# Optimization experiments

Measured on AMD Instinct MI355X. Metric: run time of the kernel, lower is better.

Reference implementation:

```python
import jax, jax.numpy as jnp
import numpy as np

# Dimensions (see shape_source): batched instruction states.
B, P, D, H, NOPS = 16384, 8, 64, 128, 37
OP_START = 16            # opcode one-hot lives in channels [16, 16+37)
DIV, MOD = 3, 4          # opcode ids for the iterative div/mod paths
CARRY_OPS = (0, 1, 2, 10, 11, 12, 13)  # ADD,SUB,MUL,LT,GT,LE,GE
NITER = 16               # div/mod iteration FFN count (source: ModuleList of 16)
NCASCADE = 7             # carry cascade iterations (source: for _ in range(7))


def setup_inputs() -> dict:
    key = jax.random.key(0)
    ks = jax.random.split(key, 20)
    s = 0.05
    n = lambda k, shape: jax.random.normal(k, shape, dtype=jnp.float32) * s
    return {
        "x": jax.random.normal(ks[0], (B, P, D), dtype=jnp.float32),
        # initial_experts (per-opcode FFN bank)
        "Wi1": n(ks[1], (NOPS, D, H)), "bi1": jnp.zeros((NOPS, H), jnp.float32),
        "Wi2": n(ks[2], (NOPS, H, D)), "bi2": jnp.zeros((NOPS, D), jnp.float32),
        # carry_attn QKV projections
        "Wq": n(ks[3], (D, D)), "Wk": n(ks[4], (D, D)), "Wv": n(ks[5], (D, D)),
        # carry_experts (per-opcode FFN bank used in the 7-iter cascade)
        "Wc1": n(ks[6], (NOPS, D, H)), "bc1": jnp.zeros((NOPS, H), jnp.float32),
        "Wc2": n(ks[7], (NOPS, H, D)), "bc2": jnp.zeros((NOPS, D), jnp.float32),
        # 16 distinct DivIterFFN layers
        "Wd1": n(ks[8], (NITER, D, H)), "bd1": jnp.zeros((NITER, H), jnp.float32),
        "Wd2": n(ks[9], (NITER, H, D)), "bd2": jnp.zeros((NITER, D), jnp.float32),
        # 16 distinct ModIterFFN layers
        "Wm1": n(ks[10], (NITER, D, H)), "bm1": jnp.zeros((NITER, H), jnp.float32),
        "Wm2": n(ks[11], (NITER, H, D)), "bm2": jnp.zeros((NITER, D), jnp.float32),
        # final_experts (per-opcode FFN bank)
        "Wf1": n(ks[12], (NOPS, D, H)), "bf1": jnp.zeros((NOPS, H), jnp.float32),
        "Wf2": n(ks[13], (NOPS, H, D)), "bf2": jnp.zeros((NOPS, D), jnp.float32),
    }


def _moe(x, op, W1, b1, W2, b2):
    """Opcode-routed expert FFN with residual: each batch element uses its opcode's weights."""
    h = jax.nn.relu(jnp.einsum('bpd,bdh->bph', x, W1[op]) + b1[op][:, None, :])
    return x + jnp.einsum('bph,bhd->bpd', h, W2[op]) + b2[op][:, None, :]


def _attn(x, Wq, Wk, Wv):
    """Carry-propagation attention across the 8 nibble positions, residual."""
    q, k, v = x @ Wq, x @ Wk, x @ Wv
    s = jax.nn.softmax(jnp.einsum('bpd,bqd->bpq', q, k) * (1.0 / np.sqrt(D)), axis=-1)
    return x + jnp.einsum('bpq,bqd->bpd', s, v)


def reference(x, Wi1, bi1, Wi2, bi2, Wq, Wk, Wv, Wc1, bc1, Wc2, bc2,
              Wd1, bd1, Wd2, bd2, Wm1, bm1, Wm2, bm2, Wf1, bf1, Wf2, bf2):
    # opcode routing: argmax over the one-hot opcode slice at position 0
    op = jnp.argmax(x[:, 0, OP_START:OP_START + NOPS], axis=-1)  # [B] int
    # Stage 1: initial opcode-routed experts
    x = _moe(x, op, Wi1, bi1, Wi2, bi2)
    carry_mask = jnp.any(op[:, None] == jnp.asarray(CARRY_OPS)[None, :], axis=1)[:, None, None]
    for _ in range(NCASCADE):
        y = _moe(_attn(x, Wq, Wk, Wv), op, Wc1, bc1, Wc2, bc2)
        x = jnp.where(carry_mask, y, x)
    # 16 iterative DIV FFNs (distinct weights per iteration), masked to DIV rows
    div_mask = (op == DIV)[:, None, None]
    for i in range(NITER):
        h = jax.nn.relu(jnp.einsum('bpd,dh->bph', x, Wd1[i]) + bd1[i])
        x = jnp.where(div_mask, x + jnp.einsum('bph,hd->bpd', h, Wd2[i]) + bd2[i], x)
    # 16 iterative MOD FFNs, masked to MOD rows
    mod_mask = (op == MOD)[:, None, None]
    for i in range(NITER):
        h = jax.nn.relu(jnp.einsum('bpd,dh->bph', x, Wm1[i]) + bm1[i])
        x = jnp.where(mod_mask, x + jnp.einsum('bph,hd->bpd', h, Wm2[i]) + bm2[i], x)
    # Stage 4: finalization experts (opcode-routed)
    x = _moe(x, op, Wf1, bf1, Wf2, bf2)
    return x
```

## Files before the change

### kernel.cpp

```cpp
#include <hip/hip_runtime.h>
#include <math.h>


typedef __bf16 bfrag __attribute__((ext_vector_type(8)));
typedef float f32x4 __attribute__((ext_vector_type(4)));

#define MFMA16(a,b,c) __builtin_amdgcn_mfma_f32_16x16x32_bf16((a),(b),(c),0,0,0)

constexpr int NB = 16384, NOPS = 37, OP_START = 16;

constexpr int WS_OPARR  = 0;
constexpr int WS_CNT    = 16384;
constexpr int WS_OFF    = 16448;
constexpr int WS_CUR    = 16512;
constexpr int WS_TB     = 16560;
constexpr int WS_ROWIDX = 16640;
constexpr int WS_INTS   = 33024;

constexpr int OFF_QKVT = 0;
constexpr int OFF_WI1T = 12288;
constexpr int OFF_WI2T = 315392;
constexpr int OFF_WC1T = 618496;
constexpr int OFF_WC2T = 921600;
constexpr int OFF_WF1T = 1224704;
constexpr int OFF_WF2T = 1527808;
constexpr int OFF_WD1T = 1830912;
constexpr int OFF_WD2T = 1961984;
constexpr int OFF_WM1T = 2093056;
constexpr int OFF_WM2T = 2224128;


__global__ void k_zero(int* cnt, int* cur) {
    int t = threadIdx.x;
    if (t < NOPS) { cnt[t] = 0; cur[t] = 0; }
}

__global__ void k_op(const float* __restrict__ x, int* __restrict__ opArr, int* __restrict__ cnt) {
    int b = blockIdx.x * 64 + threadIdx.x;
    const float4* p = (const float4*)(x + (size_t)b * 512 + OP_START);
    float best = -1e30f; int op = 0;
    #pragma unroll
    for (int j = 0; j < 9; ++j) {
        float4 v = p[j];
        int k = j * 4;
        if (v.x > best) { best = v.x; op = k; }
        if (v.y > best) { best = v.y; op = k + 1; }
        if (v.z > best) { best = v.z; op = k + 2; }
        if (v.w > best) { best = v.w; op = k + 3; }
    }
    float last = x[(size_t)b * 512 + OP_START + 36];
    if (last > best) op = 36;
    opArr[b] = op;
    atomicAdd(&cnt[op], 1);
}

__global__ void k_scan(const int* __restrict__ cnt, int* __restrict__ off, int* __restrict__ tb) {
    if (threadIdx.x == 0) {
        int a = 0, t = 0;
        for (int o = 0; o < NOPS; ++o) {
            off[o] = a; a += cnt[o];
            tb[o] = t;  t += (cnt[o] + 3) >> 2;
        }
        off[NOPS] = a; tb[NOPS] = t;
    }
}

__global__ void k_scatter(const int* __restrict__ opArr, const int* __restrict__ off,
                          int* __restrict__ cur, int* __restrict__ rowIdx) {
    __shared__ int h[NOPS], bb[NOPS];
    int tid = threadIdx.x;
    if (tid < NOPS) h[tid] = 0;
    __syncthreads();
    int b = blockIdx.x * 256 + tid;
    int op = opArr[b];
    int my = atomicAdd(&h[op], 1);
    __syncthreads();
    if (tid < NOPS && h[tid] > 0) bb[tid] = atomicAdd(&cur[tid], h[tid]);
    __syncthreads();
    rowIdx[off[op] + bb[op] + my] = b;
}

__global__ void k_tilemap(const int* __restrict__ cnt, const int* __restrict__ tb,
                          int* __restrict__ tileArr) {
    int o = blockIdx.x;
    int n = (cnt[o] + 3) >> 2, base = tb[o];
    for (int t = threadIdx.x; t < n; t += 64)
        tileArr[base + t] = (o << 12) | t;
}

__global__ void k_wt(const float* __restrict__ Wi1, const float* __restrict__ Wi2,
                     const float* __restrict__ Wq,  const float* __restrict__ Wk,
                     const float* __restrict__ Wv,
                     const float* __restrict__ Wc1, const float* __restrict__ Wc2,
                     const float* __restrict__ Wd1, const float* __restrict__ Wd2,
                     const float* __restrict__ Wm1, const float* __restrict__ Wm2,
                     const float* __restrict__ Wf1, const float* __restrict__ Wf2,
                     __bf16* __restrict__ wb) {
    __shared__ float t[8320];
    int m = blockIdx.x;
    const float* src; __bf16* dst; int R, C;
    if      (m < 37)  { src = Wi1 + m * 8192;        dst = wb + OFF_WI1T + m * 8192;        R = 64;  C = 128; }
    else if (m < 74)  { src = Wi2 + (m-37) * 8192;   dst = wb + OFF_WI2T + (m-37) * 8192;   R = 128; C = 64;  }
    else if (m < 111) { src = Wc1 + (m-74) * 8192;   dst = wb + OFF_WC1T + (m-74) * 8192;   R = 64;  C = 128; }
    else if (m < 148) { src = Wc2 + (m-111) * 8192;  dst = wb + OFF_WC2T + (m-111) * 8192;  R = 128; C = 64;  }
    else if (m < 185) { src = Wf1 + (m-148) * 8192;  dst = wb + OFF_WF1T + (m-148) * 8192;  R = 64;  C = 128; }
    else if (m < 222) { src = Wf2 + (m-185) * 8192;  dst = wb + OFF_WF2T + (m-185) * 8192;  R = 128; C = 64;  }
    else if (m < 238) { src = Wd1 + (m-222) * 8192;  dst = wb + OFF_WD1T + (m-222) * 8192;  R = 64;  C = 128; }
    else if (m < 254) { src = Wd2 + (m-238) * 8192;  dst = wb + OFF_WD2T + (m-238) * 8192;  R = 128; C = 64;  }
    else if (m < 270) { src = Wm1 + (m-254) * 8192;  dst = wb + OFF_WM1T + (m-254) * 8192;  R = 64;  C = 128; }
    else if (m < 286) { src = Wm2 + (m-270) * 8192;  dst = wb + OFF_WM2T + (m-270) * 8192;  R = 128; C = 64;  }
    else { const float* q3[3] = {Wq, Wk, Wv}; src = q3[m-286]; dst = wb + OFF_QKVT + (m-286) * 4096; R = 64; C = 64; }
    int n = R * C, Cp = C + 1;
    int logC = (C == 128) ? 7 : 6, logR = (R == 128) ? 7 : 6;
    for (int i = threadIdx.x; i < n; i += 256)
        t[(i >> logC) * Cp + (i & (C - 1))] = src[i];
    __syncthreads();
    for (int o = threadIdx.x; o < n; o += 256) {
        int c = o >> logR, r = o & (R - 1);
        dst[o] = (__bf16)t[r * Cp + c];
    }
}


__device__ __forceinline__ bfrag cvt8(const float* p) {
    float4 a = *(const float4*)p;
    float4 b = *(const float4*)(p + 4);
    bfrag r;
    r[0] = (__bf16)a.x; r[1] = (__bf16)a.y; r[2] = (__bf16)a.z; r[3] = (__bf16)a.w;
    r[4] = (__bf16)b.x; r[5] = (__bf16)b.y; r[6] = (__bf16)b.z; r[7] = (__bf16)b.w;
    return r;
}

__device__ __forceinline__ bfrag zfrag() {
    bfrag r;
    #pragma unroll
    for (int j = 0; j < 8; ++j) r[j] = (__bf16)0.0f;
    return r;
}

__device__ __forceinline__ void ffn_coop(float* Xs, __bf16* Hs,
    const __bf16* __restrict__ W1t, const float* __restrict__ b1,
    const __bf16* __restrict__ W2t, const float* __restrict__ b2,
    int w, int lq, int qd) {
    __syncthreads();
    bfrag a[2][2];
    #pragma unroll
    for (int mt = 0; mt < 2; ++mt)
        #pragma unroll
        for (int kf = 0; kf < 2; ++kf)
            a[mt][kf] = cvt8(&Xs[(mt * 16 + lq) * 68 + kf * 32 + qd * 8]);
    #pragma unroll
    for (int nt2 = 0; nt2 < 2; ++nt2) {
        int nt = w * 2 + nt2;
        float bv = b1[nt * 16 + lq];
        f32x4 acc0 = {bv, bv, bv, bv}, acc1 = acc0;
        #pragma unroll
        for (int kf = 0; kf < 2; ++kf) {
            bfrag wv = *(const bfrag*)(W1t + (nt * 16 + lq) * 64 + kf * 32 + qd * 8);
            acc0 = MFMA16(a[0][kf], wv, acc0);
            acc1 = MFMA16(a[1][kf], wv, acc1);
        }
        #pragma unroll
        for (int r = 0; r < 4; ++r) {
            Hs[(qd * 4 + r) * 136 + nt * 16 + lq]      = (__bf16)fmaxf(acc0[r], 0.0f);
            Hs[(16 + qd * 4 + r) * 136 + nt * 16 + lq] = (__bf16)fmaxf(acc1[r], 0.0f);
        }
    }
    __syncthreads();
    bfrag a2[2][4];
    #pragma unroll
    for (int mt = 0; mt < 2; ++mt)
        #pragma unroll
        for (int kf = 0; kf < 4; ++kf)
            a2[mt][kf] = *(const bfrag*)&Hs[(mt * 16 + lq) * 136 + kf * 32 + qd * 8];
    {
        float bv = b2[w * 16 + lq];
        f32x4 acc0 = {bv, bv, bv, bv}, acc1 = acc0;
        #pragma unroll
        for (int kf = 0; kf < 4; ++kf) {
            bfrag wv = *(const bfrag*)(W2t + (w * 16 + lq) * 128 + kf * 32 + qd * 8);
            acc0 = MFMA16(a2[0][kf], wv, acc0);
            acc1 = MFMA16(a2[1][kf], wv, acc1);
        }
        #pragma unroll
        for (int r = 0; r < 4; ++r) {
            Xs[(qd * 4 + r) * 68 + w * 16 + lq]      += acc0[r];
            Xs[(16 + qd * 4 + r) * 68 + w * 16 + lq] += acc1[r];
        }
    }
}

__device__ __forceinline__ void attn_coop(float* Xs, __bf16* Qb, __bf16* Kb, __bf16* Vt,
    float* Sf, __bf16* Pb, const __bf16* __restrict__ qkvt, int w, int lq, int qd) {
    int c = w >> 1;
    __syncthreads();
    {
        bfrag a[2];
        #pragma unroll
        for (int kf = 0; kf < 2; ++kf)
            a[kf] = cvt8(&Xs[(c * 16 + lq) * 68 + kf * 32 + qd * 8]);
        int nt0 = (w & 1) * 6;
        #pragma unroll
        for (int i = 0; i < 6; ++i) {
            int nt = nt0 + i;
            f32x4 acc = {0.f, 0.f, 0.f, 0.f};
            #pragma unroll
            for (int kf = 0; kf < 2; ++kf) {
                bfrag wv = *(const bfrag*)(qkvt + (nt * 16 + lq) * 64 + kf * 32 + qd * 8);
                acc = MFMA16(a[kf], wv, acc);
            }
            if (nt < 4) {
                #pragma unroll
                for (int r = 0; r < 4; ++r)
                    Qb[c * 1728 + (qd * 4 + r) * 72 + nt * 16 + lq] = (__bf16)acc[r];
            } else if (nt < 8) {
                #pragma unroll
                for (int r = 0; r < 4; ++r)
                    Kb[c * 1728 + (qd * 4 + r) * 72 + (nt - 4) * 16 + lq] = (__bf16)acc[r];
            } else {
                #pragma unroll
                for (int r = 0; r < 4; ++r) {
                    int m = qd * 4 + r;
                    Vt[((c * 2 + (m >> 3)) * 64 + (nt - 8) * 16 + lq) * 8 + (m & 7)] = (__bf16)acc[r];
                }
            }
        }
    }
    __syncthreads();
    {
        int sl = w & 1;
        f32x4 acc = {0.f, 0.f, 0.f, 0.f};
        #pragma unroll
        for (int kf = 0; kf < 2; ++kf) {
            bfrag qa = *(const bfrag*)&Qb[c * 1728 + (sl * 8 + lq) * 72 + kf * 32 + qd * 8];
            bfrag kb = *(const bfrag*)&Kb[c * 1728 + (sl * 8 + lq) * 72 + kf * 32 + qd * 8];
            acc = MFMA16(qa, kb, acc);
        }
        if (qd < 2 && lq < 8) {
            #pragma unroll
            for (int r = 0; r < 4; ++r)
                Sf[(w * 8 + qd * 4 + r) * 8 + lq] = acc[r] * 0.125f;
        }
    }
    __syncthreads();
    {
        int lane = qd * 16 + lq;
        if (lane < 8) {
            const float* sp = &Sf[(w * 8 + lane) * 8];
            float t[8];
            #pragma unroll
            for (int j = 0; j < 8; ++j) t[j] = sp[j];
            float mx = t[0];
            #pragma unroll
            for (int j = 1; j < 8; ++j) mx = fmaxf(mx, t[j]);
            float sum = 0.f;
            #pragma unroll
            for (int j = 0; j < 8; ++j) { t[j] = __expf(t[j] - mx); sum += t[j]; }
            float inv = 1.0f / sum;
            bfrag pv;
            #pragma unroll
            for (int j = 0; j < 8; ++j) pv[j] = (__bf16)(t[j] * inv);
            *(bfrag*)&Pb[(w * 16 + lane) * 8] = pv;
        } else if (lane < 16) {
            *(bfrag*)&Pb[(w * 16 + lane) * 8] = zfrag();
        }
    }
    __syncthreads();
    {
        bfrag pa = zfrag();
        if (qd == 0) pa = *(const bfrag*)&Pb[(w * 16 + lq) * 8];
        #pragma unroll
        for (int nt = 0; nt < 4; ++nt) {
            bfrag vb = zfrag();
            if (qd == 0) vb = *(const bfrag*)&Vt[(w * 64 + nt * 16 + lq) * 8];
            f32x4 acc = {0.f, 0.f, 0.f, 0.f};
            acc = MFMA16(pa, vb, acc);
            if (qd < 2) {
                #pragma unroll
                for (int r = 0; r < 4; ++r)
                    Xs[(w * 8 + qd * 4 + r) * 68 + nt * 16 + lq] += acc[r];
            }
        }
    }
}


__global__ void __launch_bounds__(256, 4)
moe_main(const float* __restrict__ x, float* __restrict__ out,
         const int* __restrict__ tileArr, const int* __restrict__ tb,
         const int* __restrict__ cnt, const int* __restrict__ off,
         const int* __restrict__ rowIdx, const __bf16* __restrict__ wb,
         const float* __restrict__ bi1, const float* __restrict__ bi2,
         const float* __restrict__ bc1, const float* __restrict__ bc2,
         const float* __restrict__ bd1, const float* __restrict__ bd2,
         const float* __restrict__ bm1, const float* __restrict__ bm2,
         const float* __restrict__ bf1_, const float* __restrict__ bf2_) {
    __shared__ float Xs[32 * 68];
    __shared__ __align__(16) unsigned char UB[19968];
    __bf16* Hs = (__bf16*)UB;
    __bf16* Qb = (__bf16*)UB;
    __bf16* Kb = (__bf16*)(UB + 6912);
    __bf16* Vt = (__bf16*)(UB + 13824);
    float*  Sf = (float*)(UB + 17920);
    __bf16* Pb = (__bf16*)(UB + 18944);

    int g = blockIdx.x;
    if (g >= tb[NOPS]) return;
    int v = tileArr[g];
    int op = v >> 12, tile = v & 4095;

    int tid = threadIdx.x;
    int w = tid >> 6, lane = tid & 63, lq = lane & 15, qd = lane >> 4;

    int base = off[op] + tile * 4;
    int nr = cnt[op] - tile * 4; if (nr > 4) nr = 4;
    int rows[4];
    #pragma unroll
    for (int s = 0; s < 4; ++s) rows[s] = rowIdx[base + (s < nr ? s : nr - 1)];

    for (int i = tid; i < 2048; i += 256) {
        int m = i >> 6, d = i & 63;
        Xs[m * 68 + d] = x[(size_t)rows[m >> 3] * 512 + (m & 7) * 64 + d];
    }

    ffn_coop(Xs, Hs, wb + OFF_WI1T + op * 8192, bi1 + op * 128,
                     wb + OFF_WI2T + op * 8192, bi2 + op * 64, w, lq, qd);

    bool carry = (op <= 2) || (op >= 10 && op <= 13);
    if (carry) {
        const __bf16* qkvt = wb + OFF_QKVT;
        for (int it = 0; it < 7; ++it) {
            attn_coop(Xs, Qb, Kb, Vt, Sf, Pb, qkvt, w, lq, qd);
            ffn_coop(Xs, Hs, wb + OFF_WC1T + op * 8192, bc1 + op * 128,
                             wb + OFF_WC2T + op * 8192, bc2 + op * 64, w, lq, qd);
        }
    }
    if (op == 3) {
        for (int i = 0; i < 16; ++i)
            ffn_coop(Xs, Hs, wb + OFF_WD1T + i * 8192, bd1 + i * 128,
                             wb + OFF_WD2T + i * 8192, bd2 + i * 64, w, lq, qd);
    }
    if (op == 4) {
        for (int i = 0; i < 16; ++i)
            ffn_coop(Xs, Hs, wb + OFF_WM1T + i * 8192, bm1 + i * 128,
                             wb + OFF_WM2T + i * 8192, bm2 + i * 64, w, lq, qd);
    }
    ffn_coop(Xs, Hs, wb + OFF_WF1T + op * 8192, bf1_ + op * 128,
                     wb + OFF_WF2T + op * 8192, bf2_ + op * 64, w, lq, qd);

    __syncthreads();
    for (int i = tid; i < nr * 512; i += 256) {
        int s = i >> 9, rem = i & 511;
        out[(size_t)rows[s] * 512 + rem] = Xs[(s * 8 + (rem >> 6)) * 68 + (rem & 63)];
    }
}


extern "C" void kernel_launch(void* const* d_in, const int* in_sizes, int n_in,
                              void* d_out, int out_size, void* d_ws, size_t ws_size,
                              hipStream_t stream) {
    (void)in_sizes; (void)n_in; (void)out_size; (void)ws_size;
    const float* x   = (const float*)d_in[0];
    const float* Wi1 = (const float*)d_in[1];
    const float* bi1 = (const float*)d_in[2];
    const float* Wi2 = (const float*)d_in[3];
    const float* bi2 = (const float*)d_in[4];
    const float* Wq  = (const float*)d_in[5];
    const float* Wk  = (const float*)d_in[6];
    const float* Wv  = (const float*)d_in[7];
    const float* Wc1 = (const float*)d_in[8];
    const float* bc1 = (const float*)d_in[9];
    const float* Wc2 = (const float*)d_in[10];
    const float* bc2 = (const float*)d_in[11];
    const float* Wd1 = (const float*)d_in[12];
    const float* bd1 = (const float*)d_in[13];
    const float* Wd2 = (const float*)d_in[14];
    const float* bd2 = (const float*)d_in[15];
    const float* Wm1 = (const float*)d_in[16];
    const float* bm1 = (const float*)d_in[17];
    const float* Wm2 = (const float*)d_in[18];
    const float* bm2 = (const float*)d_in[19];
    const float* Wf1 = (const float*)d_in[20];
    const float* bf1 = (const float*)d_in[21];
    const float* Wf2 = (const float*)d_in[22];
    const float* bf2 = (const float*)d_in[23];
    float* out = (float*)d_out;

    int* wsi     = (int*)d_ws;
    int* opArr   = wsi + WS_OPARR;
    int* tileArr = wsi + WS_OPARR;
    int* cnt     = wsi + WS_CNT;
    int* off     = wsi + WS_OFF;
    int* cur     = wsi + WS_CUR;
    int* tb      = wsi + WS_TB;
    int* rowIdx  = wsi + WS_ROWIDX;
    __bf16* wb   = (__bf16*)((char*)d_ws + WS_INTS * 4);

    k_zero<<<1, 64, 0, stream>>>(cnt, cur);
    k_op<<<NB / 64, 64, 0, stream>>>(x, opArr, cnt);
    k_scan<<<1, 64, 0, stream>>>(cnt, off, tb);
    k_scatter<<<NB / 256, 256, 0, stream>>>(opArr, off, cur, rowIdx);
    k_tilemap<<<NOPS, 64, 0, stream>>>(cnt, tb, tileArr);
    k_wt<<<289, 256, 0, stream>>>(Wi1, Wi2, Wq, Wk, Wv, Wc1, Wc2, Wd1, Wd2, Wm1, Wm2, Wf1, Wf2, wb);
    moe_main<<<NB / 4 + NOPS, 256, 0, stream>>>(x, out, tileArr, tb, cnt, off, rowIdx, wb,
                                                bi1, bi2, bc1, bc2, bd1, bd2, bm1, bm2, bf1, bf2);
}
```

Before: 273.8 us.

## Schedule heavy-op tiles first, transpose MFMA operands, fuse softmax via shuffles

The tile scan now orders the costly opcodes first (DIV, MOD, then the carry ops) so the longest blocks launch early and the tail is shorter. The FFN and attention MFMAs swap operand order so each lane writes four contiguous outputs as one vector store to shared memory. Softmax is done in registers with cross-lane shuffles, removing one shared-memory pass and one barrier. Launch bounds rise to 5 blocks per CU, which adds register pressure, and the padded Pb/VtT regions must be zeroed up front.

```diff
diff --git a/kernel.cpp b/kernel.cpp
--- a/kernel.cpp
+++ b/kernel.cpp
@@ -3,6 +3,7 @@
 
 
 typedef __bf16 bfrag __attribute__((ext_vector_type(8)));
+typedef __bf16 bhalf4 __attribute__((ext_vector_type(4)));
 typedef float f32x4 __attribute__((ext_vector_type(4)));
 
 #define MFMA16(a,b,c) __builtin_amdgcn_mfma_f32_16x16x32_bf16((a),(b),(c),0,0,0)
@@ -56,12 +57,18 @@
 
 __global__ void k_scan(const int* __restrict__ cnt, int* __restrict__ off, int* __restrict__ tb) {
     if (threadIdx.x == 0) {
-        int a = 0, t = 0;
+        int a = 0;
+        for (int o = 0; o < NOPS; ++o) { off[o] = a; a += cnt[o]; }
+        off[NOPS] = a;
+        const int pr[9] = {3, 4, 0, 1, 2, 10, 11, 12, 13};
+        int t = 0;
+        for (int i = 0; i < 9; ++i) { int o = pr[i]; tb[o] = t; t += (cnt[o] + 3) >> 2; }
         for (int o = 0; o < NOPS; ++o) {
-            off[o] = a; a += cnt[o];
-            tb[o] = t;  t += (cnt[o] + 3) >> 2;
-        }
-        off[NOPS] = a; tb[NOPS] = t;
+            bool heavy = (o <= 4) || (o >= 10 && o <= 13);
+            if (heavy) continue;
+            tb[o] = t; t += (cnt[o] + 3) >> 2;
+        }
+        tb[NOPS] = t;
     }
 }
 
@@ -131,10 +138,16 @@
     return r;
 }
 
-__device__ __forceinline__ bfrag zfrag() {
-    bfrag r;
-    #pragma unroll
-    for (int j = 0; j < 8; ++j) r[j] = (__bf16)0.0f;
+__device__ __forceinline__ bhalf4 pack4(f32x4 a) {
+    bhalf4 r;
+    r[0] = (__bf16)a[0]; r[1] = (__bf16)a[1]; r[2] = (__bf16)a[2]; r[3] = (__bf16)a[3];
+    return r;
+}
+
+__device__ __forceinline__ bhalf4 pack4_relu(f32x4 a) {
+    bhalf4 r;
+    r[0] = (__bf16)fmaxf(a[0], 0.0f); r[1] = (__bf16)fmaxf(a[1], 0.0f);
+    r[2] = (__bf16)fmaxf(a[2], 0.0f); r[3] = (__bf16)fmaxf(a[3], 0.0f);
     return r;
 }
 
@@ -143,149 +156,134 @@
     const __bf16* __restrict__ W2t, const float* __restrict__ b2,
     int w, int lq, int qd) {
     __syncthreads();
-    bfrag a[2][2];
-    #pragma unroll
-    for (int mt = 0; mt < 2; ++mt)
+    {
+        bfrag xa[2][2];
+        #pragma unroll
+        for (int mt = 0; mt < 2; ++mt)
+            #pragma unroll
+            for (int kf = 0; kf < 2; ++kf)
+                xa[mt][kf] = cvt8(&Xs[(mt * 16 + lq) * 68 + kf * 32 + qd * 8]);
+        #pragma unroll
+        for (int nt2 = 0; nt2 < 2; ++nt2) {
+            int nt = w * 2 + nt2;
+            float4 bv = *(const float4*)(b1 + nt * 16 + qd * 4);
+            f32x4 acc0 = {bv.x, bv.y, bv.z, bv.w}, acc1 = acc0;
+            #pragma unroll
+            for (int kf = 0; kf < 2; ++kf) {
+                bfrag wf = *(const bfrag*)(W1t + (nt * 16 + lq) * 64 + kf * 32 + qd * 8);
+                acc0 = MFMA16(wf, xa[0][kf], acc0);
+                acc1 = MFMA16(wf, xa[1][kf], acc1);
+            }
+            *(bhalf4*)&Hs[lq * 136 + nt * 16 + qd * 4]        = pack4_relu(acc0);
+            *(bhalf4*)&Hs[(16 + lq) * 136 + nt * 16 + qd * 4] = pack4_relu(acc1);
+        }
+    }
+    __syncthreads();
+    {
+        float4 bv = *(const float4*)(b2 + w * 16 + qd * 4);
+        f32x4 acc0 = {bv.x, bv.y, bv.z, bv.w}, acc1 = acc0;
+        #pragma unroll
+        for (int kf = 0; kf < 4; ++kf) {
+            bfrag wf = *(const bfrag*)(W2t + (w * 16 + lq) * 128 + kf * 32 + qd * 8);
+            bfrag h0 = *(const bfrag*)&Hs[lq * 136 + kf * 32 + qd * 8];
+            bfrag h1 = *(const bfrag*)&Hs[(16 + lq) * 136 + kf * 32 + qd * 8];
+            acc0 = MFMA16(wf, h0, acc0);
+            acc1 = MFMA16(wf, h1, acc1);
+        }
+        float4* p0 = (float4*)&Xs[lq * 68 + w * 16 + qd * 4];
+        float4 v0 = *p0;
+        v0.x += acc0[0]; v0.y += acc0[1]; v0.z += acc0[2]; v0.w += acc0[3];
+        *p0 = v0;
+        float4* p1 = (float4*)&Xs[(16 + lq) * 68 + w * 16 + qd * 4];
+        float4 v1 = *p1;
+        v1.x += acc1[0]; v1.y += acc1[1]; v1.z += acc1[2]; v1.w += acc1[3];
+        *p1 = v1;
+    }
+}
+
+__device__ __forceinline__ void attn_coop(float* Xs, __bf16* Qb, __bf16* Kb,
+    __bf16* VtT, __bf16* Pb, const __bf16* __restrict__ qkvt, int w, int lq, int qd) {
+    int c = w >> 1, half = w & 1;
+    __syncthreads();
+    {
+        bfrag xa[2];
         #pragma unroll
         for (int kf = 0; kf < 2; ++kf)
-            a[mt][kf] = cvt8(&Xs[(mt * 16 + lq) * 68 + kf * 32 + qd * 8]);
-    #pragma unroll
-    for (int nt2 = 0; nt2 < 2; ++nt2) {
-        int nt = w * 2 + nt2;
-        float bv = b1[nt * 16 + lq];
-        f32x4 acc0 = {bv, bv, bv, bv}, acc1 = acc0;
-        #pragma unroll
-        for (int kf = 0; kf < 2; ++kf) {
-            bfrag wv = *(const bfrag*)(W1t + (nt * 16 + lq) * 64 + kf * 32 + qd * 8);
-            acc0 = MFMA16(a[0][kf], wv, acc0);
-            acc1 = MFMA16(a[1][kf], wv, acc1);
-        }
-        #pragma unroll
-        for (int r = 0; r < 4; ++r) {
-            Hs[(qd * 4 + r) * 136 + nt * 16 + lq]      = (__bf16)fmaxf(acc0[r], 0.0f);
-            Hs[(16 + qd * 4 + r) * 136 + nt * 16 + lq] = (__bf16)fmaxf(acc1[r], 0.0f);
-        }
-    }
-    __syncthreads();
-    bfrag a2[2][4];
-    #pragma unroll
-    for (int mt = 0; mt < 2; ++mt)
-        #pragma unroll
-        for (int kf = 0; kf < 4; ++kf)
-            a2[mt][kf] = *(const bfrag*)&Hs[(mt * 16 + lq) * 136 + kf * 32 + qd * 8];
-    {
-        float bv = b2[w * 16 + lq];
-        f32x4 acc0 = {bv, bv, bv, bv}, acc1 = acc0;
-        #pragma unroll
-        for (int kf = 0; kf < 4; ++kf) {
-            bfrag wv = *(const bfrag*)(W2t + (w * 16 + lq) * 128 + kf * 32 + qd * 8);
-            acc0 = MFMA16(a2[0][kf], wv, acc0);
-            acc1 = MFMA16(a2[1][kf], wv, acc1);
-        }
-        #pragma unroll
-        for (int r = 0; r < 4; ++r) {
-            Xs[(qd * 4 + r) * 68 + w * 16 + lq]      += acc0[r];
-            Xs[(16 + qd * 4 + r) * 68 + w * 16 + lq] += acc1[r];
-        }
-    }
-}
-
-__device__ __forceinline__ void attn_coop(float* Xs, __bf16* Qb, __bf16* Kb, __bf16* Vt,
-    float* Sf, __bf16* Pb, const __bf16* __restrict__ qkvt, int w, int lq, int qd) {
-    int c = w >> 1;
-    __syncthreads();
-    {
-        bfrag a[2];
-        #pragma unroll
-        for (int kf = 0; kf < 2; ++kf)
-            a[kf] = cvt8(&Xs[(c * 16 + lq) * 68 + kf * 32 + qd * 8]);
-        int nt0 = (w & 1) * 6;
+            xa[kf] = cvt8(&Xs[(c * 16 + lq) * 68 + kf * 32 + qd * 8]);
+        int nt0 = half * 6;
         #pragma unroll
         for (int i = 0; i < 6; ++i) {
             int nt = nt0 + i;
             f32x4 acc = {0.f, 0.f, 0.f, 0.f};
-            #pragma unroll
-            for (int kf = 0; kf < 2; ++kf) {
-                bfrag wv = *(const bfrag*)(qkvt + (nt * 16 + lq) * 64 + kf * 32 + qd * 8);
-                acc = MFMA16(a[kf], wv, acc);
-            }
-            if (nt < 4) {
+            if (nt < 8) {
                 #pragma unroll
-                for (int r = 0; r < 4; ++r)
-                    Qb[c * 1728 + (qd * 4 + r) * 72 + nt * 16 + lq] = (__bf16)acc[r];
-            } else if (nt < 8) {
-                #pragma unroll
-                for (int r = 0; r < 4; ++r)
-                    Kb[c * 1728 + (qd * 4 + r) * 72 + (nt - 4) * 16 + lq] = (__bf16)acc[r];
+                for (int kf = 0; kf < 2; ++kf) {
+                    bfrag wf = *(const bfrag*)(qkvt + (nt * 16 + lq) * 64 + kf * 32 + qd * 8);
+                    acc = MFMA16(wf, xa[kf], acc);
+                }
+                __bf16* dst = (nt < 4)
+                    ? &Qb[c * 1280 + lq * 80 + nt * 16 + qd * 4]
+                    : &Kb[c * 1280 + lq * 80 + (nt - 4) * 16 + qd * 4];
+                *(bhalf4*)dst = pack4(acc);
             } else {
                 #pragma unroll
-                for (int r = 0; r < 4; ++r) {
-                    int m = qd * 4 + r;
-                    Vt[((c * 2 + (m >> 3)) * 64 + (nt - 8) * 16 + lq) * 8 + (m & 7)] = (__bf16)acc[r];
+                for (int kf = 0; kf < 2; ++kf) {
+                    bfrag wf = *(const bfrag*)(qkvt + (nt * 16 + lq) * 64 + kf * 32 + qd * 8);
+                    acc = MFMA16(xa[kf], wf, acc);
                 }
+                *(bhalf4*)&VtT[c * 2048 + ((nt - 8) * 16 + lq) * 32 + qd * 4] = pack4(acc);
             }
         }
     }
     __syncthreads();
     {
-        int sl = w & 1;
-        f32x4 acc = {0.f, 0.f, 0.f, 0.f};
+        f32x4 sv = {0.f, 0.f, 0.f, 0.f};
         #pragma unroll
         for (int kf = 0; kf < 2; ++kf) {
-            bfrag qa = *(const bfrag*)&Qb[c * 1728 + (sl * 8 + lq) * 72 + kf * 32 + qd * 8];
-            bfrag kb = *(const bfrag*)&Kb[c * 1728 + (sl * 8 + lq) * 72 + kf * 32 + qd * 8];
-            acc = MFMA16(qa, kb, acc);
-        }
-        if (qd < 2 && lq < 8) {
+            bfrag qa = *(const bfrag*)&Qb[c * 1280 + (half * 8 + lq) * 80 + kf * 32 + qd * 8];
+            bfrag kb = *(const bfrag*)&Kb[c * 1280 + (half * 8 + lq) * 80 + kf * 32 + qd * 8];
+            sv = MFMA16(qa, kb, sv);
+        }
+        float p4[4];
+        #pragma unroll
+        for (int r = 0; r < 4; ++r) {
+            float v = sv[r] * 0.125f;
+            float m = v;
+            m = fmaxf(m, __shfl_xor(m, 1));
+            m = fmaxf(m, __shfl_xor(m, 2));
+            m = fmaxf(m, __shfl_xor(m, 4));
+            float e = __expf(v - m);
+            float s = e;
+            s += __shfl_xor(s, 1);
+            s += __shfl_xor(s, 2);
+            s += __shfl_xor(s, 4);
+            p4[r] = e * __builtin_amdgcn_rcpf(s);
+        }
+        if (lq < 8 && qd < 2) {
             #pragma unroll
             for (int r = 0; r < 4; ++r)
-                Sf[(w * 8 + qd * 4 + r) * 8 + lq] = acc[r] * 0.125f;
+                Pb[c * 512 + (half * 8 + qd * 4 + r) * 32 + half * 8 + lq] = (__bf16)p4[r];
         }
     }
     __syncthreads();
     {
-        int lane = qd * 16 + lq;
-        if (lane < 8) {
-            const float* sp = &Sf[(w * 8 + lane) * 8];
-            float t[8];
-            #pragma unroll
-            for (int j = 0; j < 8; ++j) t[j] = sp[j];
-            float mx = t[0];
-            #pragma unroll
-            for (int j = 1; j < 8; ++j) mx = fmaxf(mx, t[j]);
-            float sum = 0.f;
-            #pragma unroll
-            for (int j = 0; j < 8; ++j) { t[j] = __expf(t[j] - mx); sum += t[j]; }
-            float inv = 1.0f / sum;
-            bfrag pv;
-            #pragma unroll
-            for (int j = 0; j < 8; ++j) pv[j] = (__bf16)(t[j] * inv);
-            *(bfrag*)&Pb[(w * 16 + lane) * 8] = pv;
-        } else if (lane < 16) {
-            *(bfrag*)&Pb[(w * 16 + lane) * 8] = zfrag();
-        }
-    }
-    __syncthreads();
-    {
-        bfrag pa = zfrag();
-        if (qd == 0) pa = *(const bfrag*)&Pb[(w * 16 + lq) * 8];
-        #pragma unroll
-        for (int nt = 0; nt < 4; ++nt) {
-            bfrag vb = zfrag();
-            if (qd == 0) vb = *(const bfrag*)&Vt[(w * 64 + nt * 16 + lq) * 8];
-            f32x4 acc = {0.f, 0.f, 0.f, 0.f};
-            acc = MFMA16(pa, vb, acc);
-            if (qd < 2) {
-                #pragma unroll
-                for (int r = 0; r < 4; ++r)
-                    Xs[(w * 8 + qd * 4 + r) * 68 + nt * 16 + lq] += acc[r];
-            }
-        }
-    }
-}
-
-
-__global__ void __launch_bounds__(256, 4)
+        bfrag pb = *(const bfrag*)&Pb[c * 512 + lq * 32 + qd * 8];
+        #pragma unroll
+        for (int i = 0; i < 2; ++i) {
+            int nt = half * 2 + i;
+            bfrag va = *(const bfrag*)&VtT[c * 2048 + (nt * 16 + lq) * 32 + qd * 8];
+            f32x4 z = {0.f, 0.f, 0.f, 0.f};
+            f32x4 acc = MFMA16(va, pb, z);
+            float4* xp = (float4*)&Xs[(c * 16 + lq) * 68 + nt * 16 + qd * 4];
+            float4 xv = *xp;
+            xv.x += acc[0]; xv.y += acc[1]; xv.z += acc[2]; xv.w += acc[3];
+            *xp = xv;
+        }
+    }
+}
+
+
+__global__ void __launch_bounds__(256, 5)
 moe_main(const float* __restrict__ x, float* __restrict__ out,
          const int* __restrict__ tileArr, const int* __restrict__ tb,
          const int* __restrict__ cnt, const int* __restrict__ off,
@@ -296,13 +294,12 @@
          const float* __restrict__ bm1, const float* __restrict__ bm2,
          const float* __restrict__ bf1_, const float* __restrict__ bf2_) {
     __shared__ float Xs[32 * 68];
-    __shared__ __align__(16) unsigned char UB[19968];
-    __bf16* Hs = (__bf16*)UB;
-    __bf16* Qb = (__bf16*)UB;
-    __bf16* Kb = (__bf16*)(UB + 6912);
-    __bf16* Vt = (__bf16*)(UB + 13824);
-    float*  Sf = (float*)(UB + 17920);
-    __bf16* Pb = (__bf16*)(UB + 18944);
+    __shared__ __align__(16) unsigned char UB[20480];
+    __bf16* Hs  = (__bf16*)UB;
+    __bf16* Qb  = (__bf16*)UB;
+    __bf16* Kb  = (__bf16*)(UB + 5120);
+    __bf16* VtT = (__bf16*)(UB + 10240);
+    __bf16* Pb  = (__bf16*)(UB + 18432);
 
     int g = blockIdx.x;
     if (g >= tb[NOPS]) return;
@@ -318,19 +315,27 @@
     #pragma unroll
     for (int s = 0; s < 4; ++s) rows[s] = rowIdx[base + (s < nr ? s : nr - 1)];
 
+    bool carry = (op <= 2) || (op >= 10 && op <= 13);
+
     for (int i = tid; i < 2048; i += 256) {
         int m = i >> 6, d = i & 63;
         Xs[m * 68 + d] = x[(size_t)rows[m >> 3] * 512 + (m & 7) * 64 + d];
     }
+    if (carry) {
+        for (int i = tid; i < 1024; i += 256) Pb[i] = (__bf16)0.0f;
+        for (int i = tid; i < 2048; i += 256) {
+            int c2 = i >> 10, rem = i & 1023, d = rem >> 4, p = rem & 15;
+            VtT[c2 * 2048 + d * 32 + 16 + p] = (__bf16)0.0f;
+        }
+    }
 
     ffn_coop(Xs, Hs, wb + OFF_WI1T + op * 8192, bi1 + op * 128,
                      wb + OFF_WI2T + op * 8192, bi2 + op * 64, w, lq, qd);
 
-    bool carry = (op <= 2) || (op >= 10 && op <= 13);
     if (carry) {
         const __bf16* qkvt = wb + OFF_QKVT;
         for (int it = 0; it < 7; ++it) {
-            attn_coop(Xs, Qb, Kb, Vt, Sf, Pb, qkvt, w, lq, qd);
+            attn_coop(Xs, Qb, Kb, VtT, Pb, qkvt, w, lq, qd);
             ffn_coop(Xs, Hs, wb + OFF_WC1T + op * 8192, bc1 + op * 128,
                              wb + OFF_WC2T + op * 8192, bc2 + op * 64, w, lq, qd);
         }
```

New measurement: 292.1 us. 6.7% more time.
